# Kernel optimization log

Measured on AMD Instinct MI355X. Metric: run time of the kernel, lower is better.

Reference implementation:

```python
import jax, jax.numpy as jnp
import numpy as np

N = 50000   # nodes
E = 800000  # edges (avg degree 16)
D = 128     # in_features == out_features (residual)
NEG_SLOPE = 0.2
BN_EPS = 1e-5


def setup_inputs() -> dict:
    key = jax.random.key(0)
    ks = jax.random.split(key, 8)
    x = jax.random.normal(ks[0], (N, D), jnp.float32)
    edge_index = jax.random.randint(ks[1], (2, E), 0, N, dtype=jnp.int32)
    W = jax.random.normal(ks[2], (D, D), jnp.float32) * 0.05
    att_src = jax.random.normal(ks[3], (D,), jnp.float32) * 0.1
    att_dst = jax.random.normal(ks[4], (D,), jnp.float32) * 0.1
    bias = jax.random.normal(ks[5], (D,), jnp.float32) * 0.01
    gamma = jnp.ones((D,), jnp.float32) + jax.random.normal(ks[6], (D,), jnp.float32) * 0.05
    beta = jax.random.normal(ks[7], (D,), jnp.float32) * 0.05
    return {"x": x, "edge_index": edge_index, "W": W, "att_src": att_src,
            "att_dst": att_dst, "bias": bias, "gamma": gamma, "beta": beta}


def reference(x, edge_index, W, att_src, att_dst, bias, gamma, beta):
    src, dst = edge_index[0], edge_index[1]
    # Linear transform (GATConv lin)
    h = x @ W                                   # [N, D]
    # Per-node attention logit halves
    a_s = h @ att_src                           # [N]
    a_d = h @ att_dst                           # [N]
    # Per-edge logits + LeakyReLU
    e = jax.nn.leaky_relu(a_s[src] + a_d[dst], NEG_SLOPE)  # [E]
    # Segment softmax over destination neighborhoods
    m = jax.ops.segment_max(e, dst, num_segments=N)        # [N]
    m = jnp.where(jnp.isfinite(m), m, 0.0)
    p = jnp.exp(e - m[dst])                                 # [E]
    denom = jax.ops.segment_sum(p, dst, num_segments=N)    # [N]
    alpha = p / denom[dst]                                  # [E]
    # Scatter-aggregate weighted neighbor features
    y = jax.ops.segment_sum(alpha[:, None] * h[src], dst, num_segments=N)  # [N, D]
    y = y + bias
    # NormDropRes (eval mode): BN with running_mean=0, running_var=1; dropout off
    yn = gamma * (y / jnp.sqrt(1.0 + BN_EPS)) + beta
    yn = jax.nn.relu(yn)
    # residual: in==out so base = x
    return x + yn
```

## Files before the change

### kernel.cpp

```cpp
#include <hip/hip_runtime.h>
#include <math.h>

#define NN 50000
#define EE 800000
#define DD 128
#define NEG 0.2f
#define SLOT 48
#define NWIN 128
#define WIN 391
#define CAP 7168

typedef short bf16x8 __attribute__((ext_vector_type(8)));
typedef float f32x4  __attribute__((ext_vector_type(4)));
typedef int   i32x4  __attribute__((ext_vector_type(4)));

__device__ __forceinline__ unsigned short f2bf(float f) {
    unsigned u = __float_as_uint(f);
    unsigned r = u + 0x7fffu + ((u >> 16) & 1u);
    return (unsigned short)(r >> 16);
}

__global__ __launch_bounds__(256) void k_init(
        const float* __restrict__ W, unsigned short* __restrict__ wt,
        const int* __restrict__ ei,
        int* __restrict__ win_cnt, unsigned* __restrict__ pairs)
{
    const int t = threadIdx.x;
    if (blockIdx.x < 64) {
        int idx = blockIdx.x * 256 + t;
        int k = idx >> 7, n = idx & 127;
        wt[n * DD + k] = f2bf(W[idx]);
        return;
    }

    __shared__ int lcnt[NWIN];
    __shared__ int lbase[NWIN];
    if (t < NWIN) lcnt[t] = 0;
    __syncthreads();

    int idx = (int)(blockIdx.x - 64) * 256 + t;
    int b[4], lp[4];
    unsigned v[4];
    bool valid = idx < EE / 4;
    if (valid) {
        i32x4 s4 = __builtin_nontemporal_load(&((const i32x4*)ei)[idx]);
        i32x4 d4 = __builtin_nontemporal_load(&((const i32x4*)(ei + EE))[idx]);
        b[0] = d4.x / WIN; v[0] = ((unsigned)(d4.x - b[0] * WIN) << 16) | (unsigned)s4.x;
        b[1] = d4.y / WIN; v[1] = ((unsigned)(d4.y - b[1] * WIN) << 16) | (unsigned)s4.y;
        b[2] = d4.z / WIN; v[2] = ((unsigned)(d4.z - b[2] * WIN) << 16) | (unsigned)s4.z;
        b[3] = d4.w / WIN; v[3] = ((unsigned)(d4.w - b[3] * WIN) << 16) | (unsigned)s4.w;
        lp[0] = atomicAdd(&lcnt[b[0]], 1);
        lp[1] = atomicAdd(&lcnt[b[1]], 1);
        lp[2] = atomicAdd(&lcnt[b[2]], 1);
        lp[3] = atomicAdd(&lcnt[b[3]], 1);
    }
    __syncthreads();
    if (t < NWIN) lbase[t] = atomicAdd(&win_cnt[t], lcnt[t]);
    __syncthreads();
    if (valid) {
#pragma unroll
        for (int k = 0; k < 4; k++) {
            int pos = lbase[b[k]] + lp[k];
            if (pos < CAP) pairs[(size_t)b[k] * CAP + pos] = v[k];
        }
    }
}

#define XS_STRIDE 136
__global__ __launch_bounds__(256) void k_fused(
        const float* __restrict__ x, const unsigned short* __restrict__ wtg,
        const float* __restrict__ att_src, const float* __restrict__ att_dst,
        unsigned short* __restrict__ hb, float* __restrict__ a_s, float* __restrict__ a_d,
        const int* __restrict__ win_cnt, const unsigned* __restrict__ pairs,
        int* __restrict__ cursor, unsigned short* __restrict__ slots)
{
    __shared__ __align__(16) short smem[26112];

    const int t = threadIdx.x;

    if (blockIdx.x & 1) {
        int w = (int)(blockIdx.x >> 1);
        if (w >= NWIN) return;
        int* lcur = (int*)smem;
        unsigned short* lslots = (unsigned short*)smem + 800;
        for (int i = t; i < 400; i += 256) lcur[i] = 0;
        __syncthreads();

        int n = win_cnt[w]; if (n > CAP) n = CAP;
        const unsigned* pw = pairs + (size_t)w * CAP;
        for (int g = t; g < n; g += 256) {
            unsigned v = pw[g];
            int ld = (int)(v >> 16);
            int pos = atomicAdd(&lcur[ld], 1);
            if (pos < SLOT) lslots[ld * SLOT + pos] = (unsigned short)(v & 0xffffu);
        }
        __syncthreads();

        const uint4* src = (const uint4*)lslots;
        uint4* dst = (uint4*)(slots + (size_t)w * WIN * SLOT);
        for (int i = t; i < WIN * SLOT / 8; i += 256) dst[i] = src[i];
        int base = w * WIN;
        for (int i = t; i < WIN; i += 256) {
            int d = base + i;
            if (d < NN) cursor[d] = lcur[i];
        }
        return;
    }

    short* xs = smem;
    short* ws = smem + 64 * XS_STRIDE;
    const int g = (int)(blockIdx.x >> 1);
    const int row0 = g * 64;

#pragma unroll
    for (int i = 0; i < 4; i++) {
        int idx = t + i * 256;
        int m = idx >> 4, c = idx & 15;
        int row = row0 + m;
        float4 f0 = make_float4(0.f, 0.f, 0.f, 0.f), f1 = f0;
        if (row < NN) {
            const float* p = x + (size_t)row * DD + c * 8;
            f0 = *(const float4*)p;
            f1 = *(const float4*)(p + 4);
        }
        bf16x8 v;
        v[0] = (short)f2bf(f0.x); v[1] = (short)f2bf(f0.y);
        v[2] = (short)f2bf(f0.z); v[3] = (short)f2bf(f0.w);
        v[4] = (short)f2bf(f1.x); v[5] = (short)f2bf(f1.y);
        v[6] = (short)f2bf(f1.z); v[7] = (short)f2bf(f1.w);
        *(bf16x8*)&xs[m * XS_STRIDE + c * 8] = v;
    }
#pragma unroll
    for (int i = 0; i < 8; i++) {
        int idx = t + i * 256;
        int n = idx >> 4, c = idx & 15;
        uint4 v = ((const uint4*)wtg)[idx];
        *(uint4*)&ws[n * XS_STRIDE + c * 8] = v;
    }
    __syncthreads();

    const int wv = t >> 6;
    const int lane = t & 63;
    const int n0 = lane & 15;
    const int quad = lane >> 4;

    bf16x8 afr[4];
#pragma unroll
    for (int kc = 0; kc < 4; kc++)
        afr[kc] = *(const bf16x8*)&xs[(wv * 16 + n0) * XS_STRIDE + kc * 32 + quad * 8];

    f32x4 acc[8];
#pragma unroll
    for (int nt = 0; nt < 8; nt++) {
        f32x4 a = {0.f, 0.f, 0.f, 0.f};
#pragma unroll
        for (int kc = 0; kc < 4; kc++) {
            bf16x8 bfr = *(const bf16x8*)&ws[(nt * 16 + n0) * XS_STRIDE + kc * 32 + quad * 8];
            a = __builtin_amdgcn_mfma_f32_16x16x32_bf16(afr[kc], bfr, a, 0, 0, 0);
        }
        acc[nt] = a;
    }

    const int rbase = row0 + wv * 16 + quad * 4;
    float ss[4] = {0.f, 0.f, 0.f, 0.f};
    float sd[4] = {0.f, 0.f, 0.f, 0.f};
#pragma unroll
    for (int nt = 0; nt < 8; nt++) {
        int col = nt * 16 + n0;
        float asc = att_src[col], adc = att_dst[col];
#pragma unroll
        for (int r = 0; r < 4; r++) {
            float v = acc[nt][r];
            ss[r] = fmaf(v, asc, ss[r]);
            sd[r] = fmaf(v, adc, sd[r]);
            int row = rbase + r;
            if (row < NN) hb[(size_t)row * DD + col] = f2bf(v);
        }
    }
#pragma unroll
    for (int r = 0; r < 4; r++) {
#pragma unroll
        for (int off = 1; off < 16; off <<= 1) {
            ss[r] += __shfl_xor(ss[r], off);
            sd[r] += __shfl_xor(sd[r], off);
        }
    }
    if (n0 == 0) {
#pragma unroll
        for (int r = 0; r < 4; r++) {
            int row = rbase + r;
            if (row < NN) { a_s[row] = ss[r]; a_d[row] = sd[r]; }
        }
    }
}

__global__ __launch_bounds__(256) void k_node(
        const int* __restrict__ cursor, const unsigned short* __restrict__ slots,
        const float* __restrict__ a_s, const float* __restrict__ a_d,
        const unsigned short* __restrict__ hb, const float* __restrict__ x,
        const float* __restrict__ bias, const float* __restrict__ gamma,
        const float* __restrict__ beta, float* __restrict__ out)
{
    int node = (int)((blockIdx.x * blockDim.x + threadIdx.x) >> 6);
    int lane = threadIdx.x & 63;
    if (node >= NN) return;

    int deg = cursor[node];
    deg = deg > SLOT ? SLOT : deg;
    float ad = a_d[node];

    int s = 0;
    float p = 0.f;
    if (lane < deg) {
        s = (int)slots[node * SLOT + lane];
        float e = a_s[s] + ad;
        e = e > 0.f ? e : NEG * e;
        p = __expf(e);
    }
    float l = p;
#pragma unroll
    for (int off = 32; off > 0; off >>= 1)
        l += __shfl_xor(l, off);

    const int eq = lane >> 4;
    const int fl = lane & 15;
    float acc[8];
#pragma unroll
    for (int k = 0; k < 8; k++) acc[k] = 0.f;

    for (int t = 0; t < deg; t += 8) {
        int i0 = t + eq, i1 = t + 4 + eq;
        int   st0 = __shfl(s, i0);
        int   st1 = __shfl(s, i1);
        float pt0 = __shfl(p, i0);
        float pt1 = __shfl(p, i1);
        uint4 hv0 = *(const uint4*)(hb + ((size_t)st0 << 7) + fl * 8);
        uint4 hv1 = *(const uint4*)(hb + ((size_t)st1 << 7) + fl * 8);
        acc[0] = fmaf(pt0, __uint_as_float(hv0.x << 16),          acc[0]);
        acc[1] = fmaf(pt0, __uint_as_float(hv0.x & 0xffff0000u),  acc[1]);
        acc[2] = fmaf(pt0, __uint_as_float(hv0.y << 16),          acc[2]);
        acc[3] = fmaf(pt0, __uint_as_float(hv0.y & 0xffff0000u),  acc[3]);
        acc[4] = fmaf(pt0, __uint_as_float(hv0.z << 16),          acc[4]);
        acc[5] = fmaf(pt0, __uint_as_float(hv0.z & 0xffff0000u),  acc[5]);
        acc[6] = fmaf(pt0, __uint_as_float(hv0.w << 16),          acc[6]);
        acc[7] = fmaf(pt0, __uint_as_float(hv0.w & 0xffff0000u),  acc[7]);
        acc[0] = fmaf(pt1, __uint_as_float(hv1.x << 16),          acc[0]);
        acc[1] = fmaf(pt1, __uint_as_float(hv1.x & 0xffff0000u),  acc[1]);
        acc[2] = fmaf(pt1, __uint_as_float(hv1.y << 16),          acc[2]);
        acc[3] = fmaf(pt1, __uint_as_float(hv1.y & 0xffff0000u),  acc[3]);
        acc[4] = fmaf(pt1, __uint_as_float(hv1.z << 16),          acc[4]);
        acc[5] = fmaf(pt1, __uint_as_float(hv1.z & 0xffff0000u),  acc[5]);
        acc[6] = fmaf(pt1, __uint_as_float(hv1.w << 16),          acc[6]);
        acc[7] = fmaf(pt1, __uint_as_float(hv1.w & 0xffff0000u),  acc[7]);
    }

#pragma unroll
    for (int off = 16; off < 64; off <<= 1) {
#pragma unroll
        for (int k = 0; k < 8; k++)
            acc[k] += __shfl_xor(acc[k], off);
    }

    if (eq == 0) {
        float invl = (deg > 0) ? 1.f / l : 0.f;
        const float invbn = 0.9999950000374997f;
        int c0 = fl * 8;
        const float* bp = bias  + c0;
        const float* gp = gamma + c0;
        const float* ep = beta  + c0;
        const float* xp = x + ((size_t)node << 7) + c0;
        float* op = out + ((size_t)node << 7) + c0;
        float4 o0, o1;
        float* oo[2] = {(float*)&o0, (float*)&o1};
#pragma unroll
        for (int k = 0; k < 8; k++) {
            float y  = acc[k] * invl + bp[k];
            float yn = gp[k] * (y * invbn) + ep[k];
            yn = yn > 0.f ? yn : 0.f;
            oo[k >> 2][k & 3] = xp[k] + yn;
        }
        *(float4*)op       = o0;
        *(float4*)(op + 4) = o1;
    }
}

extern "C" void kernel_launch(void* const* d_in, const int* in_sizes, int n_in,
                              void* d_out, int out_size, void* d_ws, size_t ws_size,
                              hipStream_t stream)
{
    const float* x     = (const float*)d_in[0];
    const int*   ei    = (const int*)  d_in[1];
    const float* W     = (const float*)d_in[2];
    const float* att_s = (const float*)d_in[3];
    const float* att_d = (const float*)d_in[4];
    const float* bias  = (const float*)d_in[5];
    const float* gamma = (const float*)d_in[6];
    const float* beta  = (const float*)d_in[7];
    float* out = (float*)d_out;

    int*            cursor  = (int*)d_ws;
    int*            win_cnt = cursor + NN;
    unsigned*       pairs   = (unsigned*)(win_cnt + NWIN);
    unsigned short* slots   = (unsigned short*)(pairs + (size_t)NWIN * CAP);
    float*          a_sv    = (float*)(slots + (size_t)NWIN * WIN * SLOT);
    float*          a_dv    = a_sv + NN;
    unsigned short* wtg     = (unsigned short*)(a_dv + NN);
    unsigned short* hb      = wtg + DD * DD;

    hipMemsetAsync(win_cnt, 0, NWIN * sizeof(int), stream);

    k_init <<<64 + (EE / 4 + 255) / 256, 256, 0, stream>>>(W, wtg, ei, win_cnt, pairs);
    k_fused<<<2 * ((NN + 63) / 64), 256, 0, stream>>>(x, wtg, att_s, att_d, hb,
                                                      a_sv, a_dv, win_cnt, pairs,
                                                      cursor, slots);
    k_node <<<(NN * 64 + 255) / 256, 256, 0, stream>>>(cursor, slots, a_sv, a_dv,
                                                        hb, x, bias, gamma, beta, out);
}
```

Before: 164.5 us.

## Pre-convert x to bf16 in init kernel and drop LDS staging in GEMM

The fp32-to-bf16 conversion of x moves out of the GEMM blocks into extra blocks of the init kernel, which write a bf16 copy of x to global memory. The GEMM blocks then read A and B fragments directly from global memory instead of staging them in LDS, which removes the shared buffer and the barrier. The aim is to cut LDS use so more blocks fit per CU and to shorten the GEMM blocks. In exchange it adds an extra global write and read of x in bf16, and B fragments are now reloaded from global or cache by every wave.

```diff
diff --git a/kernel.cpp b/kernel.cpp
--- a/kernel.cpp
+++ b/kernel.cpp
@@ -10,6 +10,10 @@
 #define WIN 391
 #define CAP 7168
 
+#define BKT_BLOCKS 782
+#define WT_BLOCKS  64
+#define CVT_BLOCKS 1563
+
 typedef short bf16x8 __attribute__((ext_vector_type(8)));
 typedef float f32x4  __attribute__((ext_vector_type(4)));
 typedef int   i32x4  __attribute__((ext_vector_type(4)));
@@ -20,16 +24,42 @@
     return (unsigned short)(r >> 16);
 }
 
+__device__ __forceinline__ bf16x8 pack8(float4 f0, float4 f1) {
+    bf16x8 v;
+    v[0] = (short)f2bf(f0.x); v[1] = (short)f2bf(f0.y);
+    v[2] = (short)f2bf(f0.z); v[3] = (short)f2bf(f0.w);
+    v[4] = (short)f2bf(f1.x); v[5] = (short)f2bf(f1.y);
+    v[6] = (short)f2bf(f1.z); v[7] = (short)f2bf(f1.w);
+    return v;
+}
+
 __global__ __launch_bounds__(256) void k_init(
         const float* __restrict__ W, unsigned short* __restrict__ wt,
+        const float* __restrict__ x, unsigned short* __restrict__ xb,
         const int* __restrict__ ei,
         int* __restrict__ win_cnt, unsigned* __restrict__ pairs)
 {
     const int t = threadIdx.x;
-    if (blockIdx.x < 64) {
-        int idx = blockIdx.x * 256 + t;
-        int k = idx >> 7, n = idx & 127;
-        wt[n * DD + k] = f2bf(W[idx]);
+    const int blk = blockIdx.x;
+
+    if (blk >= BKT_BLOCKS) {
+        if (blk < BKT_BLOCKS + WT_BLOCKS) {
+            int idx = (blk - BKT_BLOCKS) * 256 + t;
+            int k = idx >> 7, n = idx & 127;
+            wt[n * DD + k] = f2bf(W[idx]);
+        } else {
+            int g0 = (blk - BKT_BLOCKS - WT_BLOCKS) * 512 + t;
+#pragma unroll
+            for (int r = 0; r < 2; r++) {
+                int g = g0 + r * 256;
+                if (g < NN * DD / 8) {
+                    const float* p = x + (size_t)g * 8;
+                    float4 f0 = *(const float4*)p;
+                    float4 f1 = *(const float4*)(p + 4);
+                    *((bf16x8*)xb + g) = pack8(f0, f1);
+                }
+            }
+        }
         return;
     }
 
@@ -38,7 +68,7 @@
     if (t < NWIN) lcnt[t] = 0;
     __syncthreads();
 
-    int idx = (int)(blockIdx.x - 64) * 256 + t;
+    int idx = blk * 256 + t;
     int b[4], lp[4];
     unsigned v[4];
     bool valid = idx < EE / 4;
@@ -66,23 +96,20 @@
     }
 }
 
-#define XS_STRIDE 136
 __global__ __launch_bounds__(256) void k_fused(
-        const float* __restrict__ x, const unsigned short* __restrict__ wtg,
+        const unsigned short* __restrict__ xb, const unsigned short* __restrict__ wtg,
         const float* __restrict__ att_src, const float* __restrict__ att_dst,
         unsigned short* __restrict__ hb, float* __restrict__ a_s, float* __restrict__ a_d,
         const int* __restrict__ win_cnt, const unsigned* __restrict__ pairs,
         int* __restrict__ cursor, unsigned short* __restrict__ slots)
 {
-    __shared__ __align__(16) short smem[26112];
-
     const int t = threadIdx.x;
 
     if (blockIdx.x & 1) {
+        __shared__ int lcur[400];
+        __shared__ __align__(16) unsigned short lslots[WIN * SLOT];
         int w = (int)(blockIdx.x >> 1);
         if (w >= NWIN) return;
-        int* lcur = (int*)smem;
-        unsigned short* lslots = (unsigned short*)smem + 800;
         for (int i = t; i < 400; i += 256) lcur[i] = 0;
         __syncthreads();
 
@@ -107,47 +134,20 @@
         return;
     }
 
-    short* xs = smem;
-    short* ws = smem + 64 * XS_STRIDE;
     const int g = (int)(blockIdx.x >> 1);
     const int row0 = g * 64;
-
-#pragma unroll
-    for (int i = 0; i < 4; i++) {
-        int idx = t + i * 256;
-        int m = idx >> 4, c = idx & 15;
-        int row = row0 + m;
-        float4 f0 = make_float4(0.f, 0.f, 0.f, 0.f), f1 = f0;
-        if (row < NN) {
-            const float* p = x + (size_t)row * DD + c * 8;
-            f0 = *(const float4*)p;
-            f1 = *(const float4*)(p + 4);
-        }
-        bf16x8 v;
-        v[0] = (short)f2bf(f0.x); v[1] = (short)f2bf(f0.y);
-        v[2] = (short)f2bf(f0.z); v[3] = (short)f2bf(f0.w);
-        v[4] = (short)f2bf(f1.x); v[5] = (short)f2bf(f1.y);
-        v[6] = (short)f2bf(f1.z); v[7] = (short)f2bf(f1.w);
-        *(bf16x8*)&xs[m * XS_STRIDE + c * 8] = v;
-    }
-#pragma unroll
-    for (int i = 0; i < 8; i++) {
-        int idx = t + i * 256;
-        int n = idx >> 4, c = idx & 15;
-        uint4 v = ((const uint4*)wtg)[idx];
-        *(uint4*)&ws[n * XS_STRIDE + c * 8] = v;
-    }
-    __syncthreads();
-
     const int wv = t >> 6;
     const int lane = t & 63;
     const int n0 = lane & 15;
     const int quad = lane >> 4;
 
+    int arow = row0 + wv * 16 + n0;
+    int arow_c = arow < NN ? arow : NN - 1;
+
     bf16x8 afr[4];
 #pragma unroll
     for (int kc = 0; kc < 4; kc++)
-        afr[kc] = *(const bf16x8*)&xs[(wv * 16 + n0) * XS_STRIDE + kc * 32 + quad * 8];
+        afr[kc] = *(const bf16x8*)(xb + (size_t)arow_c * DD + kc * 32 + quad * 8);
 
     f32x4 acc[8];
 #pragma unroll
@@ -155,7 +155,7 @@
         f32x4 a = {0.f, 0.f, 0.f, 0.f};
 #pragma unroll
         for (int kc = 0; kc < 4; kc++) {
-            bf16x8 bfr = *(const bf16x8*)&ws[(nt * 16 + n0) * XS_STRIDE + kc * 32 + quad * 8];
+            bf16x8 bfr = *(const bf16x8*)(wtg + (size_t)(nt * 16 + n0) * DD + kc * 32 + quad * 8);
             a = __builtin_amdgcn_mfma_f32_16x16x32_bf16(afr[kc], bfr, a, 0, 0, 0);
         }
         acc[nt] = a;
@@ -305,12 +305,14 @@
     float*          a_sv    = (float*)(slots + (size_t)NWIN * WIN * SLOT);
     float*          a_dv    = a_sv + NN;
     unsigned short* wtg     = (unsigned short*)(a_dv + NN);
-    unsigned short* hb      = wtg + DD * DD;
+    unsigned short* xb      = wtg + DD * DD;
+    unsigned short* hb      = xb + (size_t)NN * DD;
 
     hipMemsetAsync(win_cnt, 0, NWIN * sizeof(int), stream);
 
-    k_init <<<64 + (EE / 4 + 255) / 256, 256, 0, stream>>>(W, wtg, ei, win_cnt, pairs);
-    k_fused<<<2 * ((NN + 63) / 64), 256, 0, stream>>>(x, wtg, att_s, att_d, hb,
+    k_init <<<BKT_BLOCKS + WT_BLOCKS + CVT_BLOCKS, 256, 0, stream>>>(
+        W, wtg, x, xb, ei, win_cnt, pairs);
+    k_fused<<<2 * ((NN + 63) / 64), 256, 0, stream>>>(xb, wtg, att_s, att_d, hb,
                                                       a_sv, a_dv, win_cnt, pairs,
                                                       cursor, slots);
     k_node <<<(NN * 64 + 255) / 256, 256, 0, stream>>>(cursor, slots, a_sv, a_dv,
```

Result: slower. 185.5 us (+12.8%).

## Overlap edge binning with GEMM and move slot fill to its own kernel

Applied to the files above, without the earlier changes.

The memset is folded into a small pre-kernel that also converts W to bf16. The edge-bucketing pass (pairs by destination window) now runs in the odd blocks of the GEMM kernel, so it overlaps the x@W work. The per-window slot scatter becomes a separate 512-thread kernel with one block per window. This removes a memset launch and lets edge binning overlap the GEMM, at the cost of an extra kernel launch and only 128 blocks in the slot-fill stage.

```diff
diff --git a/kernel.cpp b/kernel.cpp
--- a/kernel.cpp
+++ b/kernel.cpp
@@ -20,97 +20,68 @@
     return (unsigned short)(r >> 16);
 }
 
-__global__ __launch_bounds__(256) void k_init(
+__global__ __launch_bounds__(256) void k_pre(
         const float* __restrict__ W, unsigned short* __restrict__ wt,
-        const int* __restrict__ ei,
-        int* __restrict__ win_cnt, unsigned* __restrict__ pairs)
+        int* __restrict__ win_cnt)
 {
     const int t = threadIdx.x;
-    if (blockIdx.x < 64) {
-        int idx = blockIdx.x * 256 + t;
-        int k = idx >> 7, n = idx & 127;
-        wt[n * DD + k] = f2bf(W[idx]);
+    if (blockIdx.x == 64) {
+        if (t < NWIN) win_cnt[t] = 0;
         return;
     }
-
-    __shared__ int lcnt[NWIN];
-    __shared__ int lbase[NWIN];
-    if (t < NWIN) lcnt[t] = 0;
-    __syncthreads();
-
-    int idx = (int)(blockIdx.x - 64) * 256 + t;
-    int b[4], lp[4];
-    unsigned v[4];
-    bool valid = idx < EE / 4;
-    if (valid) {
-        i32x4 s4 = __builtin_nontemporal_load(&((const i32x4*)ei)[idx]);
-        i32x4 d4 = __builtin_nontemporal_load(&((const i32x4*)(ei + EE))[idx]);
-        b[0] = d4.x / WIN; v[0] = ((unsigned)(d4.x - b[0] * WIN) << 16) | (unsigned)s4.x;
-        b[1] = d4.y / WIN; v[1] = ((unsigned)(d4.y - b[1] * WIN) << 16) | (unsigned)s4.y;
-        b[2] = d4.z / WIN; v[2] = ((unsigned)(d4.z - b[2] * WIN) << 16) | (unsigned)s4.z;
-        b[3] = d4.w / WIN; v[3] = ((unsigned)(d4.w - b[3] * WIN) << 16) | (unsigned)s4.w;
-        lp[0] = atomicAdd(&lcnt[b[0]], 1);
-        lp[1] = atomicAdd(&lcnt[b[1]], 1);
-        lp[2] = atomicAdd(&lcnt[b[2]], 1);
-        lp[3] = atomicAdd(&lcnt[b[3]], 1);
-    }
-    __syncthreads();
-    if (t < NWIN) lbase[t] = atomicAdd(&win_cnt[t], lcnt[t]);
-    __syncthreads();
-    if (valid) {
-#pragma unroll
-        for (int k = 0; k < 4; k++) {
-            int pos = lbase[b[k]] + lp[k];
-            if (pos < CAP) pairs[(size_t)b[k] * CAP + pos] = v[k];
-        }
-    }
+    int idx = blockIdx.x * 256 + t;
+    int k = idx >> 7, n = idx & 127;
+    wt[n * DD + k] = f2bf(W[idx]);
 }
 
 #define XS_STRIDE 136
-__global__ __launch_bounds__(256) void k_fused(
+__global__ __launch_bounds__(256) void k_A(
         const float* __restrict__ x, const unsigned short* __restrict__ wtg,
         const float* __restrict__ att_src, const float* __restrict__ att_dst,
         unsigned short* __restrict__ hb, float* __restrict__ a_s, float* __restrict__ a_d,
-        const int* __restrict__ win_cnt, const unsigned* __restrict__ pairs,
-        int* __restrict__ cursor, unsigned short* __restrict__ slots)
+        const int* __restrict__ ei, int* __restrict__ win_cnt, unsigned* __restrict__ pairs)
 {
     __shared__ __align__(16) short smem[26112];
-
     const int t = threadIdx.x;
 
     if (blockIdx.x & 1) {
-        int w = (int)(blockIdx.x >> 1);
-        if (w >= NWIN) return;
-        int* lcur = (int*)smem;
-        unsigned short* lslots = (unsigned short*)smem + 800;
-        for (int i = t; i < 400; i += 256) lcur[i] = 0;
+        int* lcnt  = (int*)smem;
+        int* lbase = (int*)smem + NWIN;
+        if (t < NWIN) lcnt[t] = 0;
         __syncthreads();
 
-        int n = win_cnt[w]; if (n > CAP) n = CAP;
-        const unsigned* pw = pairs + (size_t)w * CAP;
-        for (int g = t; g < n; g += 256) {
-            unsigned v = pw[g];
-            int ld = (int)(v >> 16);
-            int pos = atomicAdd(&lcur[ld], 1);
-            if (pos < SLOT) lslots[ld * SLOT + pos] = (unsigned short)(v & 0xffffu);
+        int idx = (int)(blockIdx.x >> 1) * 256 + t;
+        int b[4], lp[4];
+        unsigned v[4];
+        bool valid = idx < EE / 4;
+        if (valid) {
+            i32x4 s4 = __builtin_nontemporal_load(&((const i32x4*)ei)[idx]);
+            i32x4 d4 = __builtin_nontemporal_load(&((const i32x4*)(ei + EE))[idx]);
+            b[0] = d4.x / WIN; v[0] = ((unsigned)(d4.x - b[0] * WIN) << 16) | (unsigned)s4.x;
+            b[1] = d4.y / WIN; v[1] = ((unsigned)(d4.y - b[1] * WIN) << 16) | (unsigned)s4.y;
+            b[2] = d4.z / WIN; v[2] = ((unsigned)(d4.z - b[2] * WIN) << 16) | (unsigned)s4.z;
+            b[3] = d4.w / WIN; v[3] = ((unsigned)(d4.w - b[3] * WIN) << 16) | (unsigned)s4.w;
+            lp[0] = atomicAdd(&lcnt[b[0]], 1);
+            lp[1] = atomicAdd(&lcnt[b[1]], 1);
+            lp[2] = atomicAdd(&lcnt[b[2]], 1);
+            lp[3] = atomicAdd(&lcnt[b[3]], 1);
         }
         __syncthreads();
-
-        const uint4* src = (const uint4*)lslots;
-        uint4* dst = (uint4*)(slots + (size_t)w * WIN * SLOT);
-        for (int i = t; i < WIN * SLOT / 8; i += 256) dst[i] = src[i];
-        int base = w * WIN;
-        for (int i = t; i < WIN; i += 256) {
-            int d = base + i;
-            if (d < NN) cursor[d] = lcur[i];
+        if (t < NWIN) lbase[t] = atomicAdd(&win_cnt[t], lcnt[t]);
+        __syncthreads();
+        if (valid) {
+#pragma unroll
+            for (int k = 0; k < 4; k++) {
+                int pos = lbase[b[k]] + lp[k];
+                if (pos < CAP) pairs[(size_t)b[k] * CAP + pos] = v[k];
+            }
         }
         return;
     }
 
     short* xs = smem;
     short* ws = smem + 64 * XS_STRIDE;
-    const int g = (int)(blockIdx.x >> 1);
-    const int row0 = g * 64;
+    const int row0 = (int)(blockIdx.x >> 1) * 64;
 
 #pragma unroll
     for (int i = 0; i < 4; i++) {
@@ -191,6 +162,38 @@
             int row = rbase + r;
             if (row < NN) { a_s[row] = ss[r]; a_d[row] = sd[r]; }
         }
+    }
+}
+
+__global__ __launch_bounds__(512) void k_B(
+        const int* __restrict__ win_cnt, const unsigned* __restrict__ pairs,
+        int* __restrict__ cursor, unsigned short* __restrict__ slots)
+{
+    __shared__ int lcur[400];
+    __shared__ __align__(16) unsigned short lslots[WIN * SLOT];
+    const int t = threadIdx.x;
+    const int w = blockIdx.x;
+
+    for (int i = t; i < 400; i += 512) lcur[i] = 0;
+    __syncthreads();
+
+    int n = win_cnt[w]; if (n > CAP) n = CAP;
+    const unsigned* pw = pairs + (size_t)w * CAP;
+    for (int g = t; g < n; g += 512) {
+        unsigned v = pw[g];
+        int ld = (int)(v >> 16);
+        int pos = atomicAdd(&lcur[ld], 1);
+        if (pos < SLOT) lslots[ld * SLOT + pos] = (unsigned short)(v & 0xffffu);
+    }
+    __syncthreads();
+
+    const uint4* src = (const uint4*)lslots;
+    uint4* dst = (uint4*)(slots + (size_t)w * WIN * SLOT);
+    for (int i = t; i < WIN * SLOT / 8; i += 512) dst[i] = src[i];
+    int base = w * WIN;
+    for (int i = t; i < WIN; i += 512) {
+        int d = base + i;
+        if (d < NN) cursor[d] = lcur[i];
     }
 }
 
@@ -307,12 +310,10 @@
     unsigned short* wtg     = (unsigned short*)(a_dv + NN);
     unsigned short* hb      = wtg + DD * DD;
 
-    hipMemsetAsync(win_cnt, 0, NWIN * sizeof(int), stream);
-
-    k_init <<<64 + (EE / 4 + 255) / 256, 256, 0, stream>>>(W, wtg, ei, win_cnt, pairs);
-    k_fused<<<2 * ((NN + 63) / 64), 256, 0, stream>>>(x, wtg, att_s, att_d, hb,
-                                                      a_sv, a_dv, win_cnt, pairs,
-                                                      cursor, slots);
-    k_node <<<(NN * 64 + 255) / 256, 256, 0, stream>>>(cursor, slots, a_sv, a_dv,
-                                                        hb, x, bias, gamma, beta, out);
-}
+    k_pre <<<65, 256, 0, stream>>>(W, wtg, win_cnt);
+    k_A   <<<2 * ((NN + 63) / 64), 256, 0, stream>>>(x, wtg, att_s, att_d, hb,
+                                                     a_sv, a_dv, ei, win_cnt, pairs);
+    k_B   <<<NWIN, 512, 0, stream>>>(win_cnt, pairs, cursor, slots);
+    k_node<<<(NN * 64 + 255) / 256, 256, 0, stream>>>(cursor, slots, a_sv, a_dv,
+                                                       hb, x, bias, gamma, beta, out);
+}
```

Result: faster. 158.6 us (-3.6%).
